# Kernel optimization log

Hardware: AMD Instinct MI355X
Metric: run time of the kernel (lower is better)

## Reference

```python
import jax, jax.numpy as jnp
import numpy as np

N_NODES = 100000
N_EDGES = 1600000
N_FEAT = 128
HIDDEN = 128
N_CLASSES = 10
N_GRAPHS = 512


def setup_inputs() -> dict:
    key = jax.random.key(0)
    ks = jax.random.split(key, 20)

    def lin(k, fan_in, fan_out, bias=True):
        kw, kb = jax.random.split(k)
        s = 1.0 / np.sqrt(fan_in)
        W = jax.random.uniform(kw, (fan_in, fan_out), jnp.float32, -s, s)
        if bias:
            b = jax.random.uniform(kb, (fan_out,), jnp.float32, -s, s)
            return W, b
        return W

    x = jax.random.normal(ks[0], (N_NODES, N_FEAT), jnp.float32)
    edge_index = jax.random.randint(ks[1], (2, N_EDGES), 0, N_NODES)
    batch = jnp.sort(jax.random.randint(ks[2], (N_NODES,), 0, N_GRAPHS))

    w1l, b1 = lin(ks[3], N_FEAT, HIDDEN)
    w1r = lin(ks[4], N_FEAT, HIDDEN, bias=False)
    w2l, b2 = lin(ks[5], HIDDEN, HIDDEN)
    w2r = lin(ks[6], HIDDEN, HIDDEN, bias=False)
    w3l, b3 = lin(ks[7], HIDDEN, HIDDEN)
    w3r = lin(ks[8], HIDDEN, HIDDEN, bias=False)
    gate_w, gate_b = lin(ks[9], HIDDEN, 1)
    lin1_w, lin1_b = lin(ks[10], HIDDEN, HIDDEN)
    lin2_w, lin2_b = lin(ks[11], HIDDEN, N_CLASSES)

    return dict(x=x, edge_index=edge_index, batch=batch,
                w1l=w1l, b1=b1, w1r=w1r,
                w2l=w2l, b2=b2, w2r=w2r,
                w3l=w3l, b3=b3, w3r=w3r,
                gate_w=gate_w, gate_b=gate_b,
                lin1_w=lin1_w, lin1_b=lin1_b,
                lin2_w=lin2_w, lin2_b=lin2_b)


def _sage_conv(x, src, dst, Wl, bl, Wr, n_nodes):
    # PyG SAGEConv(mean): out = lin_l(mean_{j in N(i)} x_j) + lin_r(x_i)
    msg_sum = jax.ops.segment_sum(x[src], dst, num_segments=n_nodes)
    cnt = jax.ops.segment_sum(jnp.ones((src.shape[0], 1), x.dtype), dst,
                              num_segments=n_nodes)
    mean = msg_sum / jnp.maximum(cnt, 1.0)
    return mean @ Wl + bl + x @ Wr


def reference(x, edge_index, batch,
              w1l, b1, w1r, w2l, b2, w2r, w3l, b3, w3r,
              gate_w, gate_b, lin1_w, lin1_b, lin2_w, lin2_b):
    n = x.shape[0]
    src, dst = edge_index[0], edge_index[1]

    h = jax.nn.relu(_sage_conv(x, src, dst, w1l, b1, w1r, n))
    h = jax.nn.relu(_sage_conv(h, src, dst, w2l, b2, w2r, n))
    h = jax.nn.relu(_sage_conv(h, src, dst, w3l, b3, w3r, n))

    # AttentionalAggregation: scatter-softmax of gate over graph segments
    gate = h @ gate_w + gate_b                                  # [N, 1]
    m = jax.ops.segment_max(gate, batch, num_segments=N_GRAPHS)  # [G, 1]
    e = jnp.exp(gate - m[batch])
    s = jax.ops.segment_sum(e, batch, num_segments=N_GRAPHS)     # [G, 1]
    alpha = e / s[batch]
    pooled = jax.ops.segment_sum(alpha * h, batch, num_segments=N_GRAPHS)  # [G, H]

    out = jax.nn.relu(pooled @ lin1_w + lin1_b)
    # dropout is identity in eval mode
    out = out @ lin2_w + lin2_b
    return jax.nn.log_softmax(out, axis=-1)
```

## Files before the change

kernel.cpp:

```cpp
#include <hip/hip_runtime.h>
#include <stdint.h>

#define N_NODES 100000
#define N_EDGES 1600000
#define NF 128
#define NG 512
#define NC 10

#define NBUCK ((N_NODES + 255) / 256)
#define EPB 8192

#define BSTRIDE 264

#define CVT_B 6250
#define BT_B 384
#define BOUNDS_B 3

typedef short short8 __attribute__((ext_vector_type(8)));
typedef float f32x4 __attribute__((ext_vector_type(4)));

__device__ __forceinline__ unsigned short f2b(float f) {
    unsigned u = __float_as_uint(f);
    u += 0x7fffu + ((u >> 16) & 1u);
    return (unsigned short)(u >> 16);
}
__device__ __forceinline__ float lo16(unsigned v) { return __uint_as_float(v << 16); }
__device__ __forceinline__ float hi16(unsigned v) { return __uint_as_float(v & 0xffff0000u); }

__global__ __launch_bounds__(256) void bucket_count(const int* __restrict__ dst, int* __restrict__ bcount) {
    __shared__ int h[NBUCK];
    for (int i = threadIdx.x; i < NBUCK; i += 256) h[i] = 0;
    __syncthreads();
    const int base = blockIdx.x * EPB;
    const int lim = min(base + EPB, N_EDGES);
    for (int i = base + threadIdx.x; i < lim; i += 256) atomicAdd(&h[dst[i] >> 8], 1);
    __syncthreads();
    for (int i = threadIdx.x; i < NBUCK; i += 256)
        if (h[i]) atomicAdd(&bcount[i], h[i]);
}

__global__ __launch_bounds__(512) void bucket_scan(const int* __restrict__ bcount, int* __restrict__ bbase,
                                                   int* __restrict__ gcursor, int* __restrict__ rowptr) {
    __shared__ int sh[512];
    const int t = threadIdx.x;
    int v = (t < NBUCK) ? bcount[t] : 0;
    sh[t] = v;
    __syncthreads();
    for (int off = 1; off < 512; off <<= 1) {
        int u = (t >= off) ? sh[t - off] : 0;
        __syncthreads();
        sh[t] += u;
        __syncthreads();
    }
    if (t < NBUCK) {
        int e = sh[t] - v;
        bbase[t] = e;
        gcursor[t] = e;
    }
    if (t == NBUCK - 1) bbase[NBUCK] = sh[t];
    if (t == 0) rowptr[N_NODES] = N_EDGES;
}

__global__ __launch_bounds__(256) void bucket_scatter(const int* __restrict__ src, const int* __restrict__ dst,
                                                      int* __restrict__ gcursor, unsigned* __restrict__ brec) {
    __shared__ int h[NBUCK];
    for (int i = threadIdx.x; i < NBUCK; i += 256) h[i] = 0;
    __syncthreads();
    const int base = blockIdx.x * EPB;
    const int lim = min(base + EPB, N_EDGES);
    for (int i = base + threadIdx.x; i < lim; i += 256) atomicAdd(&h[dst[i] >> 8], 1);
    __syncthreads();
    for (int i = threadIdx.x; i < NBUCK; i += 256) {
        int c = h[i];
        if (c) h[i] = atomicAdd(&gcursor[i], c);
    }
    __syncthreads();
    for (int i = base + threadIdx.x; i < lim; i += 256) {
        int d = dst[i];
        int pos = atomicAdd(&h[d >> 8], 1);
        brec[pos] = ((unsigned)(d & 255) << 17) | (unsigned)src[i];
    }
}

__global__ __launch_bounds__(256) void bucket_fill(const unsigned* __restrict__ brec, const int* __restrict__ bbase,
                                                   int* __restrict__ rowptr, int* __restrict__ eidx) {
    __shared__ int nh[256];
    __shared__ int sc[256];
    const int b = blockIdx.x, t = threadIdx.x;
    const int beg = bbase[b], end = bbase[b + 1];
    nh[t] = 0;
    __syncthreads();
    for (int i = beg + t; i < end; i += 256) atomicAdd(&nh[brec[i] >> 17], 1);
    __syncthreads();
    int cnt = nh[t];
    sc[t] = cnt;
    __syncthreads();
    for (int off = 1; off < 256; off <<= 1) {
        int u = (t >= off) ? sc[t - off] : 0;
        __syncthreads();
        sc[t] += u;
        __syncthreads();
    }
    int excl = sc[t] - cnt;
    int node = b * 256 + t;
    if (node < N_NODES) rowptr[node] = beg + excl;
    nh[t] = beg + excl;
    __syncthreads();
    for (int i = beg + t; i < end; i += 256) {
        unsigned r = brec[i];
        int pos = atomicAdd(&nh[r >> 17], 1);
        eidx[pos] = (int)(r & 0x1FFFFu);
    }
}

__global__ __launch_bounds__(256) void prep_kernel(const float* __restrict__ x, unsigned short* __restrict__ xb,
                                                   const float* __restrict__ w1l, const float* __restrict__ w1r,
                                                   const float* __restrict__ w2l, const float* __restrict__ w2r,
                                                   const float* __restrict__ w3l, const float* __restrict__ w3r,
                                                   unsigned short* __restrict__ Bt,
                                                   const int* __restrict__ batch, int* __restrict__ gstart) {
    const int b = blockIdx.x, t = threadIdx.x;
    if (b < CVT_B) {
        int i = b * 256 + t;
        const float4* ip = (const float4*)x;
        float4 a = ip[2 * i], c = ip[2 * i + 1];
        uint4 o;
        o.x = (unsigned)f2b(a.x) | ((unsigned)f2b(a.y) << 16);
        o.y = (unsigned)f2b(a.z) | ((unsigned)f2b(a.w) << 16);
        o.z = (unsigned)f2b(c.x) | ((unsigned)f2b(c.y) << 16);
        o.w = (unsigned)f2b(c.z) | ((unsigned)f2b(c.w) << 16);
        ((uint4*)xb)[i] = o;
    } else if (b < CVT_B + BT_B) {
        int i = (b - CVT_B) * 256 + t;
        int layer = i / (128 * 256);
        int r = i % (128 * 256);
        int n = r / 256, k = r % 256;
        const float* wl = (layer == 0) ? w1l : (layer == 1) ? w2l : w3l;
        const float* wr = (layer == 0) ? w1r : (layer == 1) ? w2r : w3r;
        float v = (k < 128) ? wl[k * 128 + n] : wr[(k - 128) * 128 + n];
        Bt[i] = f2b(v);
    } else {
        int g = (b - CVT_B - BT_B) * 256 + t;
        if (g > NG) return;
        int lo = 0, hi = N_NODES;
        while (lo < hi) {
            int mid = (lo + hi) >> 1;
            if (batch[mid] < g) lo = mid + 1; else hi = mid;
        }
        gstart[g] = lo;
    }
}

__global__ __launch_bounds__(256) void agg_kernel(const unsigned short* __restrict__ F,
                                                  const int* __restrict__ rowptr,
                                                  const int* __restrict__ eidx,
                                                  unsigned short* __restrict__ M) {
    int node = blockIdx.x * 4 + (threadIdx.x >> 6);
    if (node >= N_NODES) return;
    const int lane = threadIdx.x & 63;
    const int quad = lane >> 4, ql = lane & 15;
    const int beg = rowptr[node], end = rowptr[node + 1];
    const uint4* F4 = (const uint4*)F;

    float a0 = 0.f, a1 = 0.f, a2 = 0.f, a3 = 0.f, a4 = 0.f, a5 = 0.f, a6 = 0.f, a7 = 0.f;
    int t = beg + quad;
    for (; t + 12 < end; t += 16) {
        int r0 = eidx[t];
        int r1 = eidx[t + 4];
        int r2 = eidx[t + 8];
        int r3 = eidx[t + 12];
        uint4 v0 = F4[(size_t)r0 * 16 + ql];
        uint4 v1 = F4[(size_t)r1 * 16 + ql];
        uint4 v2 = F4[(size_t)r2 * 16 + ql];
        uint4 v3 = F4[(size_t)r3 * 16 + ql];
        a0 += lo16(v0.x) + lo16(v1.x) + lo16(v2.x) + lo16(v3.x);
        a1 += hi16(v0.x) + hi16(v1.x) + hi16(v2.x) + hi16(v3.x);
        a2 += lo16(v0.y) + lo16(v1.y) + lo16(v2.y) + lo16(v3.y);
        a3 += hi16(v0.y) + hi16(v1.y) + hi16(v2.y) + hi16(v3.y);
        a4 += lo16(v0.z) + lo16(v1.z) + lo16(v2.z) + lo16(v3.z);
        a5 += hi16(v0.z) + hi16(v1.z) + hi16(v2.z) + hi16(v3.z);
        a6 += lo16(v0.w) + lo16(v1.w) + lo16(v2.w) + lo16(v3.w);
        a7 += hi16(v0.w) + hi16(v1.w) + hi16(v2.w) + hi16(v3.w);
    }
    for (; t < end; t += 4) {
        uint4 v0 = F4[(size_t)eidx[t] * 16 + ql];
        a0 += lo16(v0.x); a1 += hi16(v0.x);
        a2 += lo16(v0.y); a3 += hi16(v0.y);
        a4 += lo16(v0.z); a5 += hi16(v0.z);
        a6 += lo16(v0.w); a7 += hi16(v0.w);
    }
    a0 += __shfl_xor(a0, 16); a0 += __shfl_xor(a0, 32);
    a1 += __shfl_xor(a1, 16); a1 += __shfl_xor(a1, 32);
    a2 += __shfl_xor(a2, 16); a2 += __shfl_xor(a2, 32);
    a3 += __shfl_xor(a3, 16); a3 += __shfl_xor(a3, 32);
    a4 += __shfl_xor(a4, 16); a4 += __shfl_xor(a4, 32);
    a5 += __shfl_xor(a5, 16); a5 += __shfl_xor(a5, 32);
    a6 += __shfl_xor(a6, 16); a6 += __shfl_xor(a6, 32);
    a7 += __shfl_xor(a7, 16); a7 += __shfl_xor(a7, 32);

    if (quad == 0) {
        float inv = 1.0f / (float)max(end - beg, 1);
        uint4 o;
        o.x = (unsigned)f2b(a0 * inv) | ((unsigned)f2b(a1 * inv) << 16);
        o.y = (unsigned)f2b(a2 * inv) | ((unsigned)f2b(a3 * inv) << 16);
        o.z = (unsigned)f2b(a4 * inv) | ((unsigned)f2b(a5 * inv) << 16);
        o.w = (unsigned)f2b(a6 * inv) | ((unsigned)f2b(a7 * inv) << 16);
        ((uint4*)M)[(size_t)node * 16 + ql] = o;
    }
}

__global__ __launch_bounds__(256, 2) void gemm_kernel(const unsigned short* __restrict__ Am,
                                                      const unsigned short* __restrict__ Ax,
                                                      const unsigned short* __restrict__ Bt,
                                                      const float* __restrict__ bias,
                                                      unsigned short* __restrict__ Out,
                                                      const float* __restrict__ gatew,
                                                      const float* __restrict__ gateb,
                                                      float* __restrict__ gate) {
    const int t = threadIdx.x;
    const int wave = t >> 6, lane = t & 63;
    const int lrow = lane & 15, quad = lane >> 4;
    const int row0 = blockIdx.x * 64 + wave * 16;

    __shared__ __attribute__((aligned(16))) unsigned short Bs[128 * BSTRIDE];

#pragma unroll
    for (int i = 0; i < 16; ++i) {
        int u = t + i * 256;
        int r = u >> 5, seg = u & 31;
        *(uint4*)(Bs + r * BSTRIDE + seg * 8) = *(const uint4*)(Bt + r * 256 + seg * 8);
    }
    __syncthreads();

    int arow = row0 + lrow;
    if (arow > N_NODES - 1) arow = N_NODES - 1;

    f32x4 acc[8];
#pragma unroll
    for (int nt = 0; nt < 8; ++nt) acc[nt] = (f32x4){0.f, 0.f, 0.f, 0.f};

#pragma unroll
    for (int c = 0; c < 8; ++c) {
        const unsigned short* Aarr = (c < 4) ? Am : Ax;
        const int kb = (c & 3) * 32 + quad * 8;
        short8 af = *(const short8*)(Aarr + (size_t)arow * 128 + kb);
        const int kf = c * 32 + quad * 8;
#pragma unroll
        for (int nt = 0; nt < 8; ++nt) {
            short8 bf = *(const short8*)(Bs + (nt * 16 + lrow) * BSTRIDE + kf);
            acc[nt] = __builtin_amdgcn_mfma_f32_16x16x32_bf16(af, bf, acc[nt], 0, 0, 0);
        }
    }

    float gpart[4] = {0.f, 0.f, 0.f, 0.f};
#pragma unroll
    for (int nt = 0; nt < 8; ++nt) {
        int col = nt * 16 + lrow;
        float bc = bias[col];
        float gw = gatew ? gatew[col] : 0.f;
#pragma unroll
        for (int r = 0; r < 4; ++r) {
            int row = row0 + quad * 4 + r;
            if (row < N_NODES) {
                float v = fmaxf(acc[nt][r] + bc, 0.f);
                Out[(size_t)row * 128 + col] = f2b(v);
                gpart[r] += v * gw;
            }
        }
    }
    if (gatew) {
#pragma unroll
        for (int r = 0; r < 4; ++r) {
            gpart[r] += __shfl_xor(gpart[r], 1);
            gpart[r] += __shfl_xor(gpart[r], 2);
            gpart[r] += __shfl_xor(gpart[r], 4);
            gpart[r] += __shfl_xor(gpart[r], 8);
        }
        if (lrow == 0) {
            float gb = gateb[0];
#pragma unroll
            for (int r = 0; r < 4; ++r) {
                int row = row0 + quad * 4 + r;
                if (row < N_NODES) gate[row] = gpart[r] + gb;
            }
        }
    }
}

__global__ __launch_bounds__(256) void pool_mlp_kernel(const unsigned short* __restrict__ h,
                                                       const float* __restrict__ gate,
                                                       const int* __restrict__ gstart,
                                                       const float* __restrict__ l1w,
                                                       const float* __restrict__ l1b,
                                                       const float* __restrict__ l2w,
                                                       const float* __restrict__ l2b,
                                                       float* __restrict__ out) {
    int wv = threadIdx.x >> 6;
    int g = blockIdx.x * 4 + wv;
    int lane = threadIdx.x & 63;
    __shared__ float pooled_s[4][128];
    __shared__ float hid_s[4][128];
    if (g >= NG) return;

    int beg = gstart[g], end = gstart[g + 1];

    float m = -INFINITY;
    for (int i = beg + lane; i < end; i += 64) m = fmaxf(m, gate[i]);
#pragma unroll
    for (int o = 32; o; o >>= 1) m = fmaxf(m, __shfl_xor(m, o));
    float s = 0.f;
    for (int i = beg + lane; i < end; i += 64) s += expf(gate[i] - m);
#pragma unroll
    for (int o = 32; o; o >>= 1) s += __shfl_xor(s, o);
    float invs = (s > 0.f) ? 1.0f / s : 0.f;

    float ax = 0.f, ay = 0.f;
    const unsigned* hb = (const unsigned*)h;
    int i = beg;
    for (; i + 2 <= end; i += 2) {
        float w0 = expf(gate[i] - m) * invs;
        float w1 = expf(gate[i + 1] - m) * invs;
        unsigned v0 = hb[(size_t)i * 64 + lane];
        unsigned v1 = hb[(size_t)(i + 1) * 64 + lane];
        ax += w0 * lo16(v0) + w1 * lo16(v1);
        ay += w0 * hi16(v0) + w1 * hi16(v1);
    }
    for (; i < end; ++i) {
        float w = expf(gate[i] - m) * invs;
        unsigned v = hb[(size_t)i * 64 + lane];
        ax += w * lo16(v);
        ay += w * hi16(v);
    }
    pooled_s[wv][2 * lane] = ax;
    pooled_s[wv][2 * lane + 1] = ay;

    float h0 = l1b[lane], h1 = l1b[lane + 64];
    for (int k = 0; k < 128; ++k) {
        float pv = pooled_s[wv][k];
        h0 += pv * l1w[k * 128 + lane];
        h1 += pv * l1w[k * 128 + lane + 64];
    }
    hid_s[wv][lane] = fmaxf(h0, 0.f);
    hid_s[wv][lane + 64] = fmaxf(h1, 0.f);

    float o10 = 0.f;
    if (lane < NC) {
        o10 = l2b[lane];
        for (int k = 0; k < 128; ++k) o10 += hid_s[wv][k] * l2w[k * NC + lane];
    }
    float mm = -INFINITY;
#pragma unroll
    for (int j = 0; j < NC; ++j) mm = fmaxf(mm, __shfl(o10, j));
    float ss = 0.f;
#pragma unroll
    for (int j = 0; j < NC; ++j) ss += expf(__shfl(o10, j) - mm);
    float lse = mm + logf(ss);
    if (lane < NC) out[g * NC + lane] = o10 - lse;
}

extern "C" void kernel_launch(void* const* d_in, const int* in_sizes, int n_in,
                              void* d_out, int out_size, void* d_ws, size_t ws_size,
                              hipStream_t stream) {
    const float* x   = (const float*)d_in[0];
    const int* ei    = (const int*)d_in[1];
    const int* batch = (const int*)d_in[2];
    const float* w1l = (const float*)d_in[3];
    const float* b1  = (const float*)d_in[4];
    const float* w1r = (const float*)d_in[5];
    const float* w2l = (const float*)d_in[6];
    const float* b2  = (const float*)d_in[7];
    const float* w2r = (const float*)d_in[8];
    const float* w3l = (const float*)d_in[9];
    const float* b3  = (const float*)d_in[10];
    const float* w3r = (const float*)d_in[11];
    const float* gw  = (const float*)d_in[12];
    const float* gb  = (const float*)d_in[13];
    const float* l1w = (const float*)d_in[14];
    const float* l1b = (const float*)d_in[15];
    const float* l2w = (const float*)d_in[16];
    const float* l2b = (const float*)d_in[17];
    float* out = (float*)d_out;

    const int* src = ei;
    const int* dst = ei + N_EDGES;

    char* base = (char*)d_ws;
    size_t off = 0;
    auto carve = [&](size_t bytes) -> void* {
        void* r = base + off;
        off = (off + bytes + 255) & ~(size_t)255;
        return r;
    };
    int* rowptr         = (int*)carve((size_t)(N_NODES + 1) * 4);
    int* eidx           = (int*)carve((size_t)N_EDGES * 4);
    unsigned short* Bt  = (unsigned short*)carve((size_t)3 * 128 * 256 * 2);
    unsigned short* xb  = (unsigned short*)carve((size_t)N_NODES * NF * 2);
    unsigned short* mn  = (unsigned short*)carve((size_t)N_NODES * NF * 2);
    unsigned short* hA  = (unsigned short*)carve((size_t)N_NODES * NF * 2);
    unsigned short* hB  = (unsigned short*)carve((size_t)N_NODES * NF * 2);
    float* gate         = (float*)carve((size_t)N_NODES * 4);
    int* gstart         = (int*)carve(513 * 4);
    int* bcount         = (int*)carve((NBUCK + 1) * 4);
    int* bbase          = (int*)carve((NBUCK + 1) * 4);
    int* gcursor        = (int*)carve((NBUCK + 1) * 4);
    unsigned* brec      = (unsigned*)mn;

    hipMemsetAsync(bcount, 0, (size_t)NBUCK * 4, stream);

    const int BUCK_B = (N_EDGES + EPB - 1) / EPB;
    bucket_count<<<BUCK_B, 256, 0, stream>>>(dst, bcount);
    bucket_scan<<<1, 512, 0, stream>>>(bcount, bbase, gcursor, rowptr);
    bucket_scatter<<<BUCK_B, 256, 0, stream>>>(src, dst, gcursor, brec);
    bucket_fill<<<NBUCK, 256, 0, stream>>>(brec, bbase, rowptr, eidx);

    prep_kernel<<<CVT_B + BT_B + BOUNDS_B, 256, 0, stream>>>(x, xb, w1l, w1r, w2l, w2r, w3l, w3r,
                                                             Bt, batch, gstart);

    const int AGG_B = (N_NODES + 3) / 4;
    const int GEMM_B = (N_NODES + 63) / 64;

    agg_kernel<<<AGG_B, 256, 0, stream>>>(xb, rowptr, eidx, mn);
    gemm_kernel<<<GEMM_B, 256, 0, stream>>>(mn, xb, Bt, b1, hA, nullptr, nullptr, nullptr);
    agg_kernel<<<AGG_B, 256, 0, stream>>>(hA, rowptr, eidx, mn);
    gemm_kernel<<<GEMM_B, 256, 0, stream>>>(mn, hA, Bt + 32768, b2, hB, nullptr, nullptr, nullptr);
    agg_kernel<<<AGG_B, 256, 0, stream>>>(hB, rowptr, eidx, mn);
    gemm_kernel<<<GEMM_B, 256, 0, stream>>>(mn, hB, Bt + 65536, b3, hA, gw, gb, gate);

    pool_mlp_kernel<<<(NG + 3) / 4, 256, 0, stream>>>(hA, gate, gstart, l1w, l1b, l2w, l2b, out);
}
```

Measured before the change: 521.7 us.

## Fold bucket count into prep kernel and enlarge GEMM row tile per wave

Measured after the change: 507.0 us. 1.03x faster.

```diff
diff --git a/kernel.cpp b/kernel.cpp
--- a/kernel.cpp
+++ b/kernel.cpp
@@ -15,6 +15,7 @@
 #define CVT_B 6250
 #define BT_B 384
 #define BOUNDS_B 3
+#define COUNT_B ((N_EDGES + EPB - 1) / EPB)
 
 typedef short short8 __attribute__((ext_vector_type(8)));
 typedef float f32x4 __attribute__((ext_vector_type(4)));
@@ -26,99 +27,14 @@
 }
 __device__ __forceinline__ float lo16(unsigned v) { return __uint_as_float(v << 16); }
 __device__ __forceinline__ float hi16(unsigned v) { return __uint_as_float(v & 0xffff0000u); }
-
-__global__ __launch_bounds__(256) void bucket_count(const int* __restrict__ dst, int* __restrict__ bcount) {
-    __shared__ int h[NBUCK];
-    for (int i = threadIdx.x; i < NBUCK; i += 256) h[i] = 0;
-    __syncthreads();
-    const int base = blockIdx.x * EPB;
-    const int lim = min(base + EPB, N_EDGES);
-    for (int i = base + threadIdx.x; i < lim; i += 256) atomicAdd(&h[dst[i] >> 8], 1);
-    __syncthreads();
-    for (int i = threadIdx.x; i < NBUCK; i += 256)
-        if (h[i]) atomicAdd(&bcount[i], h[i]);
-}
-
-__global__ __launch_bounds__(512) void bucket_scan(const int* __restrict__ bcount, int* __restrict__ bbase,
-                                                   int* __restrict__ gcursor, int* __restrict__ rowptr) {
-    __shared__ int sh[512];
-    const int t = threadIdx.x;
-    int v = (t < NBUCK) ? bcount[t] : 0;
-    sh[t] = v;
-    __syncthreads();
-    for (int off = 1; off < 512; off <<= 1) {
-        int u = (t >= off) ? sh[t - off] : 0;
-        __syncthreads();
-        sh[t] += u;
-        __syncthreads();
-    }
-    if (t < NBUCK) {
-        int e = sh[t] - v;
-        bbase[t] = e;
-        gcursor[t] = e;
-    }
-    if (t == NBUCK - 1) bbase[NBUCK] = sh[t];
-    if (t == 0) rowptr[N_NODES] = N_EDGES;
-}
-
-__global__ __launch_bounds__(256) void bucket_scatter(const int* __restrict__ src, const int* __restrict__ dst,
-                                                      int* __restrict__ gcursor, unsigned* __restrict__ brec) {
-    __shared__ int h[NBUCK];
-    for (int i = threadIdx.x; i < NBUCK; i += 256) h[i] = 0;
-    __syncthreads();
-    const int base = blockIdx.x * EPB;
-    const int lim = min(base + EPB, N_EDGES);
-    for (int i = base + threadIdx.x; i < lim; i += 256) atomicAdd(&h[dst[i] >> 8], 1);
-    __syncthreads();
-    for (int i = threadIdx.x; i < NBUCK; i += 256) {
-        int c = h[i];
-        if (c) h[i] = atomicAdd(&gcursor[i], c);
-    }
-    __syncthreads();
-    for (int i = base + threadIdx.x; i < lim; i += 256) {
-        int d = dst[i];
-        int pos = atomicAdd(&h[d >> 8], 1);
-        brec[pos] = ((unsigned)(d & 255) << 17) | (unsigned)src[i];
-    }
-}
-
-__global__ __launch_bounds__(256) void bucket_fill(const unsigned* __restrict__ brec, const int* __restrict__ bbase,
-                                                   int* __restrict__ rowptr, int* __restrict__ eidx) {
-    __shared__ int nh[256];
-    __shared__ int sc[256];
-    const int b = blockIdx.x, t = threadIdx.x;
-    const int beg = bbase[b], end = bbase[b + 1];
-    nh[t] = 0;
-    __syncthreads();
-    for (int i = beg + t; i < end; i += 256) atomicAdd(&nh[brec[i] >> 17], 1);
-    __syncthreads();
-    int cnt = nh[t];
-    sc[t] = cnt;
-    __syncthreads();
-    for (int off = 1; off < 256; off <<= 1) {
-        int u = (t >= off) ? sc[t - off] : 0;
-        __syncthreads();
-        sc[t] += u;
-        __syncthreads();
-    }
-    int excl = sc[t] - cnt;
-    int node = b * 256 + t;
-    if (node < N_NODES) rowptr[node] = beg + excl;
-    nh[t] = beg + excl;
-    __syncthreads();
-    for (int i = beg + t; i < end; i += 256) {
-        unsigned r = brec[i];
-        int pos = atomicAdd(&nh[r >> 17], 1);
-        eidx[pos] = (int)(r & 0x1FFFFu);
-    }
-}
 
 __global__ __launch_bounds__(256) void prep_kernel(const float* __restrict__ x, unsigned short* __restrict__ xb,
                                                    const float* __restrict__ w1l, const float* __restrict__ w1r,
                                                    const float* __restrict__ w2l, const float* __restrict__ w2r,
                                                    const float* __restrict__ w3l, const float* __restrict__ w3r,
                                                    unsigned short* __restrict__ Bt,
-                                                   const int* __restrict__ batch, int* __restrict__ gstart) {
+                                                   const int* __restrict__ batch, int* __restrict__ gstart,
+                                                   const int* __restrict__ dst, int* __restrict__ bcount) {
     const int b = blockIdx.x, t = threadIdx.x;
     if (b < CVT_B) {
         int i = b * 256 + t;
@@ -139,7 +55,7 @@
         const float* wr = (layer == 0) ? w1r : (layer == 1) ? w2r : w3r;
         float v = (k < 128) ? wl[k * 128 + n] : wr[(k - 128) * 128 + n];
         Bt[i] = f2b(v);
-    } else {
+    } else if (b < CVT_B + BT_B + BOUNDS_B) {
         int g = (b - CVT_B - BT_B) * 256 + t;
         if (g > NG) return;
         int lo = 0, hi = N_NODES;
@@ -148,6 +64,90 @@
             if (batch[mid] < g) lo = mid + 1; else hi = mid;
         }
         gstart[g] = lo;
+    } else {
+        __shared__ int h[NBUCK];
+        for (int i = t; i < NBUCK; i += 256) h[i] = 0;
+        __syncthreads();
+        const int base = (b - CVT_B - BT_B - BOUNDS_B) * EPB;
+        const int lim = min(base + EPB, N_EDGES);
+        for (int i = base + t; i < lim; i += 256) atomicAdd(&h[dst[i] >> 8], 1);
+        __syncthreads();
+        for (int i = t; i < NBUCK; i += 256)
+            if (h[i]) atomicAdd(&bcount[i], h[i]);
+    }
+}
+
+__global__ __launch_bounds__(512) void bucket_scan(const int* __restrict__ bcount, int* __restrict__ bbase,
+                                                   int* __restrict__ gcursor, int* __restrict__ rowptr) {
+    __shared__ int sh[512];
+    const int t = threadIdx.x;
+    int v = (t < NBUCK) ? bcount[t] : 0;
+    sh[t] = v;
+    __syncthreads();
+    for (int off = 1; off < 512; off <<= 1) {
+        int u = (t >= off) ? sh[t - off] : 0;
+        __syncthreads();
+        sh[t] += u;
+        __syncthreads();
+    }
+    if (t < NBUCK) {
+        int e = sh[t] - v;
+        bbase[t] = e;
+        gcursor[t] = e;
+    }
+    if (t == NBUCK - 1) bbase[NBUCK] = sh[t];
+    if (t == 0) rowptr[N_NODES] = N_EDGES;
+}
+
+__global__ __launch_bounds__(256) void bucket_scatter(const int* __restrict__ src, const int* __restrict__ dst,
+                                                      int* __restrict__ gcursor, unsigned* __restrict__ brec) {
+    __shared__ int h[NBUCK];
+    for (int i = threadIdx.x; i < NBUCK; i += 256) h[i] = 0;
+    __syncthreads();
+    const int base = blockIdx.x * EPB;
+    const int lim = min(base + EPB, N_EDGES);
+    for (int i = base + threadIdx.x; i < lim; i += 256) atomicAdd(&h[dst[i] >> 8], 1);
+    __syncthreads();
+    for (int i = threadIdx.x; i < NBUCK; i += 256) {
+        int c = h[i];
+        if (c) h[i] = atomicAdd(&gcursor[i], c);
+    }
+    __syncthreads();
+    for (int i = base + threadIdx.x; i < lim; i += 256) {
+        int d = dst[i];
+        int pos = atomicAdd(&h[d >> 8], 1);
+        brec[pos] = ((unsigned)(d & 255) << 17) | (unsigned)src[i];
+    }
+}
+
+__global__ __launch_bounds__(256) void bucket_fill(const unsigned* __restrict__ brec, const int* __restrict__ bbase,
+                                                   int* __restrict__ rowptr, int* __restrict__ eidx) {
+    __shared__ int nh[256];
+    __shared__ int sc[256];
+    const int b = blockIdx.x, t = threadIdx.x;
+    const int beg = bbase[b], end = bbase[b + 1];
+    nh[t] = 0;
+    __syncthreads();
+    for (int i = beg + t; i < end; i += 256) atomicAdd(&nh[brec[i] >> 17], 1);
+    __syncthreads();
+    int cnt = nh[t];
+    sc[t] = cnt;
+    __syncthreads();
+    for (int off = 1; off < 256; off <<= 1) {
+        int u = (t >= off) ? sc[t - off] : 0;
+        __syncthreads();
+        sc[t] += u;
+        __syncthreads();
+    }
+    int excl = sc[t] - cnt;
+    int node = b * 256 + t;
+    if (node < N_NODES) rowptr[node] = beg + excl;
+    nh[t] = beg + excl;
+    __syncthreads();
+    for (int i = beg + t; i < end; i += 256) {
+        unsigned r = brec[i];
+        int pos = atomicAdd(&nh[r >> 17], 1);
+        eidx[pos] = (int)(r & 0x1FFFFu);
     }
 }
 
@@ -220,7 +220,7 @@
     const int t = threadIdx.x;
     const int wave = t >> 6, lane = t & 63;
     const int lrow = lane & 15, quad = lane >> 4;
-    const int row0 = blockIdx.x * 64 + wave * 16;
+    const int row0 = blockIdx.x * 256 + wave * 64;
 
     __shared__ __attribute__((aligned(16))) unsigned short Bs[128 * BSTRIDE];
 
@@ -232,56 +232,73 @@
     }
     __syncthreads();
 
-    int arow = row0 + lrow;
-    if (arow > N_NODES - 1) arow = N_NODES - 1;
-
-    f32x4 acc[8];
-#pragma unroll
-    for (int nt = 0; nt < 8; ++nt) acc[nt] = (f32x4){0.f, 0.f, 0.f, 0.f};
+    f32x4 acc[4][8];
+#pragma unroll
+    for (int i = 0; i < 4; ++i)
+#pragma unroll
+        for (int j = 0; j < 8; ++j) acc[i][j] = (f32x4){0.f, 0.f, 0.f, 0.f};
 
 #pragma unroll
     for (int c = 0; c < 8; ++c) {
         const unsigned short* Aarr = (c < 4) ? Am : Ax;
         const int kb = (c & 3) * 32 + quad * 8;
-        short8 af = *(const short8*)(Aarr + (size_t)arow * 128 + kb);
         const int kf = c * 32 + quad * 8;
-#pragma unroll
-        for (int nt = 0; nt < 8; ++nt) {
-            short8 bf = *(const short8*)(Bs + (nt * 16 + lrow) * BSTRIDE + kf);
-            acc[nt] = __builtin_amdgcn_mfma_f32_16x16x32_bf16(af, bf, acc[nt], 0, 0, 0);
+        short8 af[4];
+#pragma unroll
+        for (int i = 0; i < 4; ++i) {
+            int ar = row0 + i * 16 + lrow;
+            if (ar > N_NODES - 1) ar = N_NODES - 1;
+            af[i] = *(const short8*)(Aarr + (size_t)ar * 128 + kb);
         }
-    }
-
-    float gpart[4] = {0.f, 0.f, 0.f, 0.f};
-#pragma unroll
-    for (int nt = 0; nt < 8; ++nt) {
-        int col = nt * 16 + lrow;
+#pragma unroll
+        for (int j = 0; j < 8; ++j) {
+            short8 bf = *(const short8*)(Bs + (j * 16 + lrow) * BSTRIDE + kf);
+#pragma unroll
+            for (int i = 0; i < 4; ++i)
+                acc[i][j] = __builtin_amdgcn_mfma_f32_16x16x32_bf16(af[i], bf, acc[i][j], 0, 0, 0);
+        }
+    }
+
+    float gpart[4][4];
+#pragma unroll
+    for (int i = 0; i < 4; ++i)
+#pragma unroll
+        for (int r = 0; r < 4; ++r) gpart[i][r] = 0.f;
+
+#pragma unroll
+    for (int j = 0; j < 8; ++j) {
+        int col = j * 16 + lrow;
         float bc = bias[col];
         float gw = gatew ? gatew[col] : 0.f;
 #pragma unroll
-        for (int r = 0; r < 4; ++r) {
-            int row = row0 + quad * 4 + r;
-            if (row < N_NODES) {
-                float v = fmaxf(acc[nt][r] + bc, 0.f);
-                Out[(size_t)row * 128 + col] = f2b(v);
-                gpart[r] += v * gw;
+        for (int i = 0; i < 4; ++i) {
+            int rbase = row0 + i * 16 + quad * 4;
+#pragma unroll
+            for (int r = 0; r < 4; ++r) {
+                int row = rbase + r;
+                if (row < N_NODES) {
+                    float v = fmaxf(acc[i][j][r] + bc, 0.f);
+                    Out[(size_t)row * 128 + col] = f2b(v);
+                    gpart[i][r] += v * gw;
+                }
             }
         }
     }
     if (gatew) {
-#pragma unroll
-        for (int r = 0; r < 4; ++r) {
-            gpart[r] += __shfl_xor(gpart[r], 1);
-            gpart[r] += __shfl_xor(gpart[r], 2);
-            gpart[r] += __shfl_xor(gpart[r], 4);
-            gpart[r] += __shfl_xor(gpart[r], 8);
-        }
-        if (lrow == 0) {
-            float gb = gateb[0];
+        float gb = gateb[0];
+#pragma unroll
+        for (int i = 0; i < 4; ++i) {
 #pragma unroll
             for (int r = 0; r < 4; ++r) {
-                int row = row0 + quad * 4 + r;
-                if (row < N_NODES) gate[row] = gpart[r] + gb;
+                float g = gpart[i][r];
+                g += __shfl_xor(g, 1);
+                g += __shfl_xor(g, 2);
+                g += __shfl_xor(g, 4);
+                g += __shfl_xor(g, 8);
+                if (lrow == 0) {
+                    int row = row0 + i * 16 + quad * 4 + r;
+                    if (row < N_NODES) gate[row] = g + gb;
+                }
             }
         }
     }
@@ -407,17 +424,15 @@
 
     hipMemsetAsync(bcount, 0, (size_t)NBUCK * 4, stream);
 
-    const int BUCK_B = (N_EDGES + EPB - 1) / EPB;
-    bucket_count<<<BUCK_B, 256, 0, stream>>>(dst, bcount);
+    prep_kernel<<<CVT_B + BT_B + BOUNDS_B + COUNT_B, 256, 0, stream>>>(
+        x, xb, w1l, w1r, w2l, w2r, w3l, w3r, Bt, batch, gstart, dst, bcount);
+
     bucket_scan<<<1, 512, 0, stream>>>(bcount, bbase, gcursor, rowptr);
-    bucket_scatter<<<BUCK_B, 256, 0, stream>>>(src, dst, gcursor, brec);
+    bucket_scatter<<<COUNT_B, 256, 0, stream>>>(src, dst, gcursor, brec);
     bucket_fill<<<NBUCK, 256, 0, stream>>>(brec, bbase, rowptr, eidx);
 
-    prep_kernel<<<CVT_B + BT_B + BOUNDS_B, 256, 0, stream>>>(x, xb, w1l, w1r, w2l, w2r, w3l, w3r,
-                                                             Bt, batch, gstart);
-
     const int AGG_B = (N_NODES + 3) / 4;
-    const int GEMM_B = (N_NODES + 63) / 64;
+    const int GEMM_B = (N_NODES + 255) / 256;
 
     agg_kernel<<<AGG_B, 256, 0, stream>>>(xb, rowptr, eidx, mn);
     gemm_kernel<<<GEMM_B, 256, 0, stream>>>(mn, xb, Bt, b1, hA, nullptr, nullptr, nullptr);
```
